# Kernel optimization log

Measured on AMD Instinct MI355X. Metric: run time of the kernel, lower is better.

Reference implementation:

```python
import jax, jax.numpy as jnp
import numpy as np

N_NODES = 100000
N_EDGES = 1600000
IN_DIM = 192   # n_shapes(64) * n_dims(3)
H1, H2 = 64, 32


def _glorot(key, shape):
    lim = np.sqrt(6.0 / (shape[0] + shape[1])).astype(np.float32)
    return jax.random.uniform(key, shape, jnp.float32, -lim, lim)


def setup_inputs() -> dict:
    key = jax.random.key(0)
    ks = jax.random.split(key, 8)
    verts = jax.random.normal(ks[0], (N_NODES, IN_DIM), jnp.float32)
    edges = jax.random.randint(ks[1], (N_EDGES, 2), 0, N_NODES)
    return {
        "verts": verts,
        "edges": edges,
        "W0_1": _glorot(ks[2], (IN_DIM, H1)),
        "W1_1": _glorot(ks[3], (IN_DIM, H1)),
        "b1": jnp.zeros((H1,), jnp.float32),
        "W0_2": _glorot(ks[4], (H1, H2)),
        "W1_2": _glorot(ks[5], (H1, H2)),
        "b2": jnp.zeros((H2,), jnp.float32),
    }


def cheb_conv(x, src, dst, W0, W1, b, n):
    # ChebConv K=2 with lambda_max=2: L_hat = -D^{-1/2} A D^{-1/2} (zero diagonal)
    deg = jax.ops.segment_sum(jnp.ones(src.shape, x.dtype), src, num_segments=n)
    d_inv = jnp.where(deg > 0, jax.lax.rsqrt(jnp.maximum(deg, 1.0)), 0.0)
    norm = -d_inv[src] * d_inv[dst]                      # [E]
    Tx1 = jax.ops.segment_sum(norm[:, None] * x[src], dst, num_segments=n)  # [n,F]
    return x @ W0 + Tx1 @ W1 + b


def reference(verts, edges, W0_1, W1_1, b1, W0_2, W1_2, b2):
    n = verts.shape[0]
    src, dst = edges[:, 0], edges[:, 1]  # edge_index rows after edges.t()
    x = jax.nn.relu(cheb_conv(verts, src, dst, W0_1, W1_1, b1, n))
    return cheb_conv(x, src, dst, W0_2, W1_2, b2, n)
```

## Files before the change

### kernel.cpp

```cpp
#include <hip/hip_runtime.h>

#define N_NODES 100000
#define N_EDGES 1600000
#define IN_DIM  192
#define H1      64
#define H2      32
#define NBKT    391
#define CAP_D   4608
#define K1GRID  2345

typedef __attribute__((ext_vector_type(8))) short short8;
typedef __attribute__((ext_vector_type(4))) float f32x4;

__device__ inline short f2bf(float f) {
    union { float f; unsigned u; } v; v.f = f;
    unsigned r = (v.u + 0x7FFFu + ((v.u >> 16) & 1u)) >> 16;
    return (short)r;
}
__device__ inline float bf2f(unsigned short s) {
    union { unsigned u; float f; } v; v.u = ((unsigned)s) << 16;
    return v.f;
}

__global__ __launch_bounds__(1024) void init_kernel(int* __restrict__ bucket_next) {
    int i = threadIdx.x;
    bucket_next[i] = (i & 511) * CAP_D;
}

__global__ __launch_bounds__(256) void prep_w_kernel(
    const float* __restrict__ W0_1, const float* __restrict__ W1_1,
    const float* __restrict__ W0_2, const float* __restrict__ W1_2,
    short* __restrict__ Bt1, short* __restrict__ Bt2) {
    int idx = blockIdx.x * 256 + threadIdx.x;
    if (idx < 128 * IN_DIM) {
        int n = idx / IN_DIM, k = idx % IN_DIM;
        float v = (n < H1) ? W0_1[(size_t)k * H1 + n] : W1_1[(size_t)k * H1 + (n - H1)];
        Bt1[idx] = f2bf(v);
    } else {
        int j = idx - 128 * IN_DIM;
        if (j < 64 * H1) {
            int n = j / H1, k = j % H1;
            float v = (n < H2) ? W0_2[(size_t)k * H2 + n] : W1_2[(size_t)k * H2 + (n - H2)];
            Bt2[j] = f2bf(v);
        }
    }
}

__global__ __launch_bounds__(256) void k1_fused(
    const int* __restrict__ edges, int* __restrict__ bucket_next,
    int* __restrict__ bins_dst, unsigned char* __restrict__ bins_src,
    const float* __restrict__ verts, const short* __restrict__ Bt1,
    const float* __restrict__ b1, short* __restrict__ hbase, short* __restrict__ y1b) {
    __shared__ int cntd[512];
    __shared__ int curd[512];
    __shared__ int cnts[512];
    __shared__ int curs[512];
    int b = blockIdx.x;
    int tid = threadIdx.x;
    if (b % 3 == 0) {
        int p = b / 3;
        cntd[tid] = 0; cntd[tid + 256] = 0;
        cnts[tid] = 0; cnts[tid + 256] = 0;
        __syncthreads();
        int ebase = p * 2048 + tid * 8;
        int2 ed[8]; int bd[8], bs[8];
#pragma unroll
        for (int i = 0; i < 8; ++i) {
            int e = ebase + i;
            if (e < N_EDGES) {
                ed[i] = ((const int2*)edges)[e];
                bd[i] = ed[i].y >> 8;
                bs[i] = ed[i].x >> 8;
                atomicAdd(&cntd[bd[i]], 1);
                atomicAdd(&cnts[bs[i]], 1);
            } else { bd[i] = -1; bs[i] = -1; }
        }
        __syncthreads();
        {
            int c;
            c = cntd[tid];       curd[tid]       = (c > 0) ? atomicAdd(&bucket_next[tid], c) : 0;
            c = cntd[tid + 256]; curd[tid + 256] = (c > 0) ? atomicAdd(&bucket_next[tid + 256], c) : 0;
            c = cnts[tid];       curs[tid]       = (c > 0) ? atomicAdd(&bucket_next[512 + tid], c) : 0;
            c = cnts[tid + 256]; curs[tid + 256] = (c > 0) ? atomicAdd(&bucket_next[512 + tid + 256], c) : 0;
        }
        __syncthreads();
#pragma unroll
        for (int i = 0; i < 8; ++i) {
            if (bd[i] >= 0) {
                int sd = atomicAdd(&curd[bd[i]], 1);
                if (sd < (bd[i] + 1) * CAP_D)
                    bins_dst[sd] = ((ed[i].y & 255) << 17) | ed[i].x;
                int ss = atomicAdd(&curs[bs[i]], 1);
                if (ss < (bs[i] + 1) * CAP_D)
                    bins_src[ss] = (unsigned char)(ed[i].x & 255);
            }
        }
        return;
    }
    int g = b - b / 3 - 1;
    int lane = tid & 63;
    int wave = tid >> 6;
    int rowbase = g * 64 + wave * 16;
    int lr = lane & 15;
    int lk = (lane >> 4) * 8;

    int row = rowbase + lr;
    int rc = (row < N_NODES) ? row : (N_NODES - 1);
    const float* p = verts + (size_t)rc * IN_DIM + lk;
    short8 a[6];
#pragma unroll
    for (int ks = 0; ks < 6; ++ks) {
        f32x4 u0 = *(const f32x4*)(p + ks * 32);
        f32x4 u1 = *(const f32x4*)(p + ks * 32 + 4);
        short8 t;
        t[0] = f2bf(u0[0]); t[1] = f2bf(u0[1]); t[2] = f2bf(u0[2]); t[3] = f2bf(u0[3]);
        t[4] = f2bf(u1[0]); t[5] = f2bf(u1[1]); t[6] = f2bf(u1[2]); t[7] = f2bf(u1[3]);
        a[ks] = t;
    }

    f32x4 acc[8] = {};
#pragma unroll
    for (int cf = 0; cf < 8; ++cf) {
        const short* bp = Bt1 + (size_t)(cf * 16 + lr) * IN_DIM + lk;
#pragma unroll
        for (int ks = 0; ks < 6; ++ks) {
            short8 bb = *(const short8*)(bp + ks * 32);
            acc[cf] = __builtin_amdgcn_mfma_f32_16x16x32_bf16(a[ks], bb, acc[cf], 0, 0, 0);
        }
    }

    int srow = (lane >> 4) * 4;
#pragma unroll
    for (int cf = 0; cf < 8; ++cf) {
        int colc = cf * 16 + lr;
        float bias = (colc < H1) ? b1[colc] : 0.f;
#pragma unroll
        for (int r = 0; r < 4; ++r) {
            int orow = rowbase + srow + r;
            if (orow < N_NODES) {
                float v = acc[cf][r];
                if (colc < H1) hbase[(size_t)orow * H1 + colc] = f2bf(v + bias);
                else           y1b[(size_t)orow * H1 + (colc - H1)] = f2bf(v);
            }
        }
    }
}

__global__ __launch_bounds__(256) void csr_kernel(
    const int* __restrict__ bins_dst, const unsigned char* __restrict__ bins_src,
    const int* __restrict__ bucket_next, float* __restrict__ dinv,
    int* __restrict__ row_beg, int* __restrict__ row_end, int* __restrict__ col,
    const unsigned short* __restrict__ y1b, short* __restrict__ y1s) {
    __shared__ int cnt_l[256];
    __shared__ int seg_l[256];
    __shared__ int s[256];
    __shared__ int dcnt[256];
    __shared__ float dinv_l[256];
    int b = blockIdx.x;
    int tid = threadIdx.x;
    int beg = b * CAP_D;
    int filld = bucket_next[b] - beg;
    if (filld > CAP_D) filld = CAP_D;
    int fills = bucket_next[512 + b] - beg;
    if (fills > CAP_D) fills = CAP_D;
    cnt_l[tid] = 0;
    dcnt[tid] = 0;
    __syncthreads();
    for (int i = tid; i < filld; i += 256)
        atomicAdd(&cnt_l[bins_dst[beg + i] >> 17], 1);
    for (int i = tid; i < fills; i += 256)
        atomicAdd(&dcnt[bins_src[beg + i]], 1);
    __syncthreads();
    int v = cnt_l[tid];
    s[tid] = v;
    __syncthreads();
    for (int off = 1; off < 256; off <<= 1) {
        int t = (tid >= off) ? s[tid - off] : 0;
        __syncthreads();
        s[tid] += t;
        __syncthreads();
    }
    int excl = s[tid] - v;
    seg_l[tid] = beg + excl;
    int n = b * 256 + tid;
    int d = dcnt[tid];
    float dv = (d > 0) ? rsqrtf((float)d) : 0.f;
    dinv_l[tid] = dv;
    if (n < N_NODES) {
        row_beg[n] = beg + excl;
        row_end[n] = beg + excl + v;
        dinv[n] = dv;
    }
    __syncthreads();
    for (int i = tid; i < filld; i += 256) {
        int w = bins_dst[beg + i];
        int slot = atomicAdd(&seg_l[w >> 17], 1);
        col[slot] = w & 0x1FFFF;
    }
    int nb = b * 256;
    int nmax = N_NODES - nb; if (nmax > 256) nmax = 256;
    for (int idx = tid; idx < nmax * 8; idx += 256) {
        int r = idx >> 3, j = idx & 7;
        float w = dinv_l[r];
        size_t off = (size_t)(nb + r) * H1 + j * 8;
        short8 vv = *(const short8*)&y1b[off];
        short8 o;
#pragma unroll
        for (int q = 0; q < 8; ++q) o[q] = f2bf(w * bf2f((unsigned short)vv[q]));
        *(short8*)&y1s[off] = o;
    }
}

__global__ __launch_bounds__(256) void gather1_kernel(
    const int* __restrict__ row_beg, const int* __restrict__ row_end,
    const int* __restrict__ col, const float* __restrict__ dinv,
    const unsigned short* __restrict__ hbase, const unsigned short* __restrict__ y1s,
    short* __restrict__ hb) {
    int n = blockIdx.x * 4 + (threadIdx.x >> 6);
    if (n >= N_NODES) return;
    int lane = threadIdx.x & 63;
    int beg = row_beg[n], end = row_end[n];
    float acc = 0.f;
    int i = beg;
    for (; i + 8 <= end; i += 8) {
        int s0 = col[i], s1 = col[i + 1], s2 = col[i + 2], s3 = col[i + 3];
        int s4 = col[i + 4], s5 = col[i + 5], s6 = col[i + 6], s7 = col[i + 7];
        float v0 = bf2f(y1s[(size_t)s0 * H1 + lane]);
        float v1 = bf2f(y1s[(size_t)s1 * H1 + lane]);
        float v2 = bf2f(y1s[(size_t)s2 * H1 + lane]);
        float v3 = bf2f(y1s[(size_t)s3 * H1 + lane]);
        float v4 = bf2f(y1s[(size_t)s4 * H1 + lane]);
        float v5 = bf2f(y1s[(size_t)s5 * H1 + lane]);
        float v6 = bf2f(y1s[(size_t)s6 * H1 + lane]);
        float v7 = bf2f(y1s[(size_t)s7 * H1 + lane]);
        acc += ((v0 + v1) + (v2 + v3)) + ((v4 + v5) + (v6 + v7));
    }
    for (; i + 4 <= end; i += 4) {
        int s0 = col[i], s1 = col[i + 1], s2 = col[i + 2], s3 = col[i + 3];
        float v0 = bf2f(y1s[(size_t)s0 * H1 + lane]);
        float v1 = bf2f(y1s[(size_t)s1 * H1 + lane]);
        float v2 = bf2f(y1s[(size_t)s2 * H1 + lane]);
        float v3 = bf2f(y1s[(size_t)s3 * H1 + lane]);
        acc += (v0 + v1) + (v2 + v3);
    }
    for (; i < end; ++i)
        acc += bf2f(y1s[(size_t)col[i] * H1 + lane]);
    size_t idx = (size_t)n * H1 + lane;
    float hf = bf2f(hbase[idx]) - dinv[n] * acc;
    hb[idx] = f2bf(fmaxf(hf, 0.f));
}

__global__ __launch_bounds__(256) void gemm2_mfma(
    const short* __restrict__ hb, const short* __restrict__ Bt2,
    const float* __restrict__ b2, const float* __restrict__ dinv,
    float* __restrict__ out, short* __restrict__ y2s) {
    int lane = threadIdx.x & 63;
    int wave = threadIdx.x >> 6;
    int rowbase = blockIdx.x * 128 + wave * 32;
    int lr = lane & 15;
    int lk = (lane >> 4) * 8;

    short8 a[2][2];
#pragma unroll
    for (int mr = 0; mr < 2; ++mr) {
        int row = rowbase + mr * 16 + lr;
        int rc = (row < N_NODES) ? row : (N_NODES - 1);
        const short* p = hb + (size_t)rc * H1 + lk;
        a[mr][0] = *(const short8*)(p);
        a[mr][1] = *(const short8*)(p + 32);
    }

    f32x4 acc[2][4] = {};
#pragma unroll
    for (int cf = 0; cf < 4; ++cf) {
        const short* bp = Bt2 + (size_t)(cf * 16 + lr) * H1 + lk;
#pragma unroll
        for (int ks = 0; ks < 2; ++ks) {
            short8 b = *(const short8*)(bp + ks * 32);
            acc[0][cf] = __builtin_amdgcn_mfma_f32_16x16x32_bf16(a[0][ks], b, acc[0][cf], 0, 0, 0);
            acc[1][cf] = __builtin_amdgcn_mfma_f32_16x16x32_bf16(a[1][ks], b, acc[1][cf], 0, 0, 0);
        }
    }

    int srow = (lane >> 4) * 4;
#pragma unroll
    for (int mr = 0; mr < 2; ++mr) {
#pragma unroll
        for (int cf = 0; cf < 4; ++cf) {
            int colc = cf * 16 + lr;
            float bias = (colc < H2) ? b2[colc] : 0.f;
#pragma unroll
            for (int r = 0; r < 4; ++r) {
                int row = rowbase + mr * 16 + srow + r;
                if (row < N_NODES) {
                    float v = acc[mr][cf][r];
                    if (colc < H2) out[(size_t)row * H2 + colc] = v + bias;
                    else           y2s[(size_t)row * H2 + (colc - H2)] = f2bf(dinv[row] * v);
                }
            }
        }
    }
}

__global__ __launch_bounds__(256) void gather2_kernel(
    const int* __restrict__ row_beg, const int* __restrict__ row_end,
    const int* __restrict__ col, const float* __restrict__ dinv,
    const unsigned short* __restrict__ y2s, float* __restrict__ out) {
    int wave = (blockIdx.x * 256 + threadIdx.x) >> 6;
    int lane = threadIdx.x & 63;
    int n = wave * 2 + (lane >> 5);
    if (n >= N_NODES) return;
    int c32 = lane & 31;
    int beg = row_beg[n], end = row_end[n];
    float acc = 0.f;
    int i = beg;
    for (; i + 8 <= end; i += 8) {
        int s0 = col[i], s1 = col[i + 1], s2 = col[i + 2], s3 = col[i + 3];
        int s4 = col[i + 4], s5 = col[i + 5], s6 = col[i + 6], s7 = col[i + 7];
        float v0 = bf2f(y2s[(size_t)s0 * H2 + c32]);
        float v1 = bf2f(y2s[(size_t)s1 * H2 + c32]);
        float v2 = bf2f(y2s[(size_t)s2 * H2 + c32]);
        float v3 = bf2f(y2s[(size_t)s3 * H2 + c32]);
        float v4 = bf2f(y2s[(size_t)s4 * H2 + c32]);
        float v5 = bf2f(y2s[(size_t)s5 * H2 + c32]);
        float v6 = bf2f(y2s[(size_t)s6 * H2 + c32]);
        float v7 = bf2f(y2s[(size_t)s7 * H2 + c32]);
        acc += ((v0 + v1) + (v2 + v3)) + ((v4 + v5) + (v6 + v7));
    }
    for (; i + 4 <= end; i += 4) {
        int s0 = col[i], s1 = col[i + 1], s2 = col[i + 2], s3 = col[i + 3];
        float v0 = bf2f(y2s[(size_t)s0 * H2 + c32]);
        float v1 = bf2f(y2s[(size_t)s1 * H2 + c32]);
        float v2 = bf2f(y2s[(size_t)s2 * H2 + c32]);
        float v3 = bf2f(y2s[(size_t)s3 * H2 + c32]);
        acc += (v0 + v1) + (v2 + v3);
    }
    for (; i < end; ++i)
        acc += bf2f(y2s[(size_t)col[i] * H2 + c32]);
    size_t idx = (size_t)n * H2 + c32;
    out[idx] = out[idx] - dinv[n] * acc;
}

extern "C" void kernel_launch(void* const* d_in, const int* in_sizes, int n_in,
                              void* d_out, int out_size, void* d_ws, size_t ws_size,
                              hipStream_t stream) {
    const float* verts = (const float*)d_in[0];
    const int*   edges = (const int*)  d_in[1];
    const float* W0_1  = (const float*)d_in[2];
    const float* W1_1  = (const float*)d_in[3];
    const float* b1    = (const float*)d_in[4];
    const float* W0_2  = (const float*)d_in[5];
    const float* W1_2  = (const float*)d_in[6];
    const float* b2    = (const float*)d_in[7];
    float* out = (float*)d_out;

    char* ws = (char*)d_ws;
    auto align256 = [](size_t x) { return (x + 255) & ~(size_t)255; };
    size_t o = 0;
    auto alloc = [&](size_t bytes) { size_t r = o; o = align256(o + bytes); return r; };

    int*   bucket_next = (int*)  (ws + alloc((size_t)1024 * 4));
    int*   bins_dst    = (int*)  (ws + alloc((size_t)NBKT * CAP_D * 4));
    unsigned char* bins_src = (unsigned char*)(ws + alloc((size_t)NBKT * CAP_D));
    int*   col         = (int*)  (ws + alloc((size_t)NBKT * CAP_D * 4));
    int*   row_beg     = (int*)  (ws + alloc((size_t)N_NODES * 4));
    int*   row_end     = (int*)  (ws + alloc((size_t)N_NODES * 4));
    float* dinv        = (float*)(ws + alloc((size_t)N_NODES * 4));
    short* Bt1         = (short*)(ws + alloc((size_t)128 * IN_DIM * 2));
    short* Bt2         = (short*)(ws + alloc((size_t)64 * H1 * 2));
    short* hbase       = (short*)(ws + alloc((size_t)N_NODES * H1 * 2));
    short* y1b         = (short*)(ws + alloc((size_t)N_NODES * H1 * 2));
    short* y1s         = (short*)(ws + alloc((size_t)N_NODES * H1 * 2));
    short* hb          = (short*)(ws + alloc((size_t)N_NODES * H1 * 2));
    short* y2s         = (short*)(ws + alloc((size_t)N_NODES * H2 * 2));

    init_kernel  <<<1, 1024, 0, stream>>>(bucket_next);
    prep_w_kernel<<<(128 * IN_DIM + 64 * H1 + 255) / 256, 256, 0, stream>>>(W0_1, W1_1, W0_2, W1_2, Bt1, Bt2);

    k1_fused  <<<K1GRID, 256, 0, stream>>>(edges, bucket_next, bins_dst, bins_src,
                                           verts, Bt1, b1, hbase, y1b);
    csr_kernel<<<NBKT, 256, 0, stream>>>(bins_dst, bins_src, bucket_next, dinv,
                                         row_beg, row_end, col,
                                         (const unsigned short*)y1b, y1s);

    gather1_kernel<<<(N_NODES + 3) / 4, 256, 0, stream>>>(row_beg, row_end, col, dinv,
                                                          (const unsigned short*)hbase,
                                                          (const unsigned short*)y1s, hb);
    gemm2_mfma    <<<(N_NODES + 127) / 128, 256, 0, stream>>>(hb, Bt2, b2, dinv, out, y2s);
    gather2_kernel<<<(N_NODES + 7) / 8, 256, 0, stream>>>(row_beg, row_end, col, dinv,
                                                          (const unsigned short*)y2s, out);
}
```

Baseline: 206.4 us.

## Fuse layer-1 gather with layer-2 GEMM and merge init into weight prep

Merges the first-layer neighbor gather and the second-layer MFMA GEMM into one kernel. Each block gathers 16 nodes into shared memory and immediately runs the 16x64 GEMM, which removes the hb intermediate's global write and read plus one launch. It also folds bucket initialisation into the weight-prep kernel, dropping another launch. The edge-binning blocks in k1 now each handle 8192 edges, reading edges twice rather than keeping them in registers, with fewer partition blocks interleaved among the GEMM blocks. The trade-offs are less parallelism in the binning phase and a block-wide sync between the irregular gather and the GEMM.

```diff
diff --git a/kernel.cpp b/kernel.cpp
--- a/kernel.cpp
+++ b/kernel.cpp
@@ -7,7 +7,8 @@
 #define H2      32
 #define NBKT    391
 #define CAP_D   4608
-#define K1GRID  2345
+#define NP1     196
+#define K1GRID  1759
 
 typedef __attribute__((ext_vector_type(8))) short short8;
 typedef __attribute__((ext_vector_type(4))) float f32x4;
@@ -22,15 +23,14 @@
     return v.f;
 }
 
-__global__ __launch_bounds__(1024) void init_kernel(int* __restrict__ bucket_next) {
-    int i = threadIdx.x;
-    bucket_next[i] = (i & 511) * CAP_D;
-}
-
 __global__ __launch_bounds__(256) void prep_w_kernel(
     const float* __restrict__ W0_1, const float* __restrict__ W1_1,
     const float* __restrict__ W0_2, const float* __restrict__ W1_2,
-    short* __restrict__ Bt1, short* __restrict__ Bt2) {
+    short* __restrict__ Bt1, short* __restrict__ Bt2, int* __restrict__ bucket_next) {
+    if (blockIdx.x == 0) {
+        for (int i = threadIdx.x; i < 1024; i += 256)
+            bucket_next[i] = (i & 511) * CAP_D;
+    }
     int idx = blockIdx.x * 256 + threadIdx.x;
     if (idx < 128 * IN_DIM) {
         int n = idx / IN_DIM, k = idx % IN_DIM;
@@ -57,23 +57,24 @@
     __shared__ int curs[512];
     int b = blockIdx.x;
     int tid = threadIdx.x;
-    if (b % 3 == 0) {
-        int p = b / 3;
+    if (b % 9 == 0) {
+        int p = b / 9;
         cntd[tid] = 0; cntd[tid + 256] = 0;
         cnts[tid] = 0; cnts[tid + 256] = 0;
         __syncthreads();
-        int ebase = p * 2048 + tid * 8;
-        int2 ed[8]; int bd[8], bs[8];
-#pragma unroll
-        for (int i = 0; i < 8; ++i) {
-            int e = ebase + i;
-            if (e < N_EDGES) {
-                ed[i] = ((const int2*)edges)[e];
-                bd[i] = ed[i].y >> 8;
-                bs[i] = ed[i].x >> 8;
-                atomicAdd(&cntd[bd[i]], 1);
-                atomicAdd(&cnts[bs[i]], 1);
-            } else { bd[i] = -1; bs[i] = -1; }
+        const int2* e2 = (const int2*)edges;
+        int base = p * 8192;
+        for (int c = 0; c < 4; ++c) {
+            int ebase = base + c * 2048 + tid * 8;
+#pragma unroll
+            for (int i = 0; i < 8; ++i) {
+                int e = ebase + i;
+                if (e < N_EDGES) {
+                    int2 ed = e2[e];
+                    atomicAdd(&cntd[ed.y >> 8], 1);
+                    atomicAdd(&cnts[ed.x >> 8], 1);
+                }
+            }
         }
         __syncthreads();
         {
@@ -84,20 +85,27 @@
             c = cnts[tid + 256]; curs[tid + 256] = (c > 0) ? atomicAdd(&bucket_next[512 + tid + 256], c) : 0;
         }
         __syncthreads();
-#pragma unroll
-        for (int i = 0; i < 8; ++i) {
-            if (bd[i] >= 0) {
-                int sd = atomicAdd(&curd[bd[i]], 1);
-                if (sd < (bd[i] + 1) * CAP_D)
-                    bins_dst[sd] = ((ed[i].y & 255) << 17) | ed[i].x;
-                int ss = atomicAdd(&curs[bs[i]], 1);
-                if (ss < (bs[i] + 1) * CAP_D)
-                    bins_src[ss] = (unsigned char)(ed[i].x & 255);
+        for (int c = 0; c < 4; ++c) {
+            int ebase = base + c * 2048 + tid * 8;
+#pragma unroll
+            for (int i = 0; i < 8; ++i) {
+                int e = ebase + i;
+                if (e < N_EDGES) {
+                    int2 ed = e2[e];
+                    int bd = ed.y >> 8;
+                    int sd = atomicAdd(&curd[bd], 1);
+                    if (sd < (bd + 1) * CAP_D)
+                        bins_dst[sd] = ((ed.y & 255) << 17) | ed.x;
+                    int bs = ed.x >> 8;
+                    int ss = atomicAdd(&curs[bs], 1);
+                    if (ss < (bs + 1) * CAP_D)
+                        bins_src[ss] = (unsigned char)(ed.x & 255);
+                }
             }
         }
         return;
     }
-    int g = b - b / 3 - 1;
+    int g = b - b / 9 - 1;
     int lane = tid & 63;
     int wave = tid >> 6;
     int rowbase = g * 64 + wave * 16;
@@ -211,94 +219,66 @@
     }
 }
 
-__global__ __launch_bounds__(256) void gather1_kernel(
+__global__ __launch_bounds__(256) void g1g2_kernel(
     const int* __restrict__ row_beg, const int* __restrict__ row_end,
     const int* __restrict__ col, const float* __restrict__ dinv,
     const unsigned short* __restrict__ hbase, const unsigned short* __restrict__ y1s,
-    short* __restrict__ hb) {
-    int n = blockIdx.x * 4 + (threadIdx.x >> 6);
-    if (n >= N_NODES) return;
-    int lane = threadIdx.x & 63;
-    int beg = row_beg[n], end = row_end[n];
-    float acc = 0.f;
-    int i = beg;
-    for (; i + 8 <= end; i += 8) {
-        int s0 = col[i], s1 = col[i + 1], s2 = col[i + 2], s3 = col[i + 3];
-        int s4 = col[i + 4], s5 = col[i + 5], s6 = col[i + 6], s7 = col[i + 7];
-        float v0 = bf2f(y1s[(size_t)s0 * H1 + lane]);
-        float v1 = bf2f(y1s[(size_t)s1 * H1 + lane]);
-        float v2 = bf2f(y1s[(size_t)s2 * H1 + lane]);
-        float v3 = bf2f(y1s[(size_t)s3 * H1 + lane]);
-        float v4 = bf2f(y1s[(size_t)s4 * H1 + lane]);
-        float v5 = bf2f(y1s[(size_t)s5 * H1 + lane]);
-        float v6 = bf2f(y1s[(size_t)s6 * H1 + lane]);
-        float v7 = bf2f(y1s[(size_t)s7 * H1 + lane]);
-        acc += ((v0 + v1) + (v2 + v3)) + ((v4 + v5) + (v6 + v7));
-    }
-    for (; i + 4 <= end; i += 4) {
-        int s0 = col[i], s1 = col[i + 1], s2 = col[i + 2], s3 = col[i + 3];
-        float v0 = bf2f(y1s[(size_t)s0 * H1 + lane]);
-        float v1 = bf2f(y1s[(size_t)s1 * H1 + lane]);
-        float v2 = bf2f(y1s[(size_t)s2 * H1 + lane]);
-        float v3 = bf2f(y1s[(size_t)s3 * H1 + lane]);
-        acc += (v0 + v1) + (v2 + v3);
-    }
-    for (; i < end; ++i)
-        acc += bf2f(y1s[(size_t)col[i] * H1 + lane]);
-    size_t idx = (size_t)n * H1 + lane;
-    float hf = bf2f(hbase[idx]) - dinv[n] * acc;
-    hb[idx] = f2bf(fmaxf(hf, 0.f));
-}
-
-__global__ __launch_bounds__(256) void gemm2_mfma(
-    const short* __restrict__ hb, const short* __restrict__ Bt2,
-    const float* __restrict__ b2, const float* __restrict__ dinv,
+    const short* __restrict__ Bt2, const float* __restrict__ b2,
     float* __restrict__ out, short* __restrict__ y2s) {
-    int lane = threadIdx.x & 63;
-    int wave = threadIdx.x >> 6;
-    int rowbase = blockIdx.x * 128 + wave * 32;
+    __shared__ short hb_l[16][68];
+    int tid = threadIdx.x, lane = tid & 63, wv = tid >> 6;
+    int nb = blockIdx.x * 16;
+    for (int j = 0; j < 4; ++j) {
+        int n = nb + wv * 4 + j;
+        int beg = row_beg[n], end = row_end[n];
+        float acc = 0.f;
+        int i = beg;
+        for (; i + 8 <= end; i += 8) {
+            int s0 = col[i], s1 = col[i + 1], s2 = col[i + 2], s3 = col[i + 3];
+            int s4 = col[i + 4], s5 = col[i + 5], s6 = col[i + 6], s7 = col[i + 7];
+            float v0 = bf2f(y1s[(size_t)s0 * H1 + lane]);
+            float v1 = bf2f(y1s[(size_t)s1 * H1 + lane]);
+            float v2 = bf2f(y1s[(size_t)s2 * H1 + lane]);
+            float v3 = bf2f(y1s[(size_t)s3 * H1 + lane]);
+            float v4 = bf2f(y1s[(size_t)s4 * H1 + lane]);
+            float v5 = bf2f(y1s[(size_t)s5 * H1 + lane]);
+            float v6 = bf2f(y1s[(size_t)s6 * H1 + lane]);
+            float v7 = bf2f(y1s[(size_t)s7 * H1 + lane]);
+            acc += ((v0 + v1) + (v2 + v3)) + ((v4 + v5) + (v6 + v7));
+        }
+        for (; i + 4 <= end; i += 4) {
+            int s0 = col[i], s1 = col[i + 1], s2 = col[i + 2], s3 = col[i + 3];
+            float v0 = bf2f(y1s[(size_t)s0 * H1 + lane]);
+            float v1 = bf2f(y1s[(size_t)s1 * H1 + lane]);
+            float v2 = bf2f(y1s[(size_t)s2 * H1 + lane]);
+            float v3 = bf2f(y1s[(size_t)s3 * H1 + lane]);
+            acc += (v0 + v1) + (v2 + v3);
+        }
+        for (; i < end; ++i)
+            acc += bf2f(y1s[(size_t)col[i] * H1 + lane]);
+        float hf = bf2f(hbase[(size_t)n * H1 + lane]) - dinv[n] * acc;
+        hb_l[wv * 4 + j][lane] = f2bf(fmaxf(hf, 0.f));
+    }
+    __syncthreads();
     int lr = lane & 15;
     int lk = (lane >> 4) * 8;
-
-    short8 a[2][2];
-#pragma unroll
-    for (int mr = 0; mr < 2; ++mr) {
-        int row = rowbase + mr * 16 + lr;
-        int rc = (row < N_NODES) ? row : (N_NODES - 1);
-        const short* p = hb + (size_t)rc * H1 + lk;
-        a[mr][0] = *(const short8*)(p);
-        a[mr][1] = *(const short8*)(p + 32);
-    }
-
-    f32x4 acc[2][4] = {};
-#pragma unroll
-    for (int cf = 0; cf < 4; ++cf) {
-        const short* bp = Bt2 + (size_t)(cf * 16 + lr) * H1 + lk;
-#pragma unroll
-        for (int ks = 0; ks < 2; ++ks) {
-            short8 b = *(const short8*)(bp + ks * 32);
-            acc[0][cf] = __builtin_amdgcn_mfma_f32_16x16x32_bf16(a[0][ks], b, acc[0][cf], 0, 0, 0);
-            acc[1][cf] = __builtin_amdgcn_mfma_f32_16x16x32_bf16(a[1][ks], b, acc[1][cf], 0, 0, 0);
-        }
-    }
-
+    short8 a0 = *(const short8*)&hb_l[lr][lk];
+    short8 a1 = *(const short8*)&hb_l[lr][32 + lk];
+    const short* bp = Bt2 + (size_t)(wv * 16 + lr) * H1 + lk;
+    short8 b0 = *(const short8*)(bp);
+    short8 b1 = *(const short8*)(bp + 32);
+    f32x4 acc2 = {};
+    acc2 = __builtin_amdgcn_mfma_f32_16x16x32_bf16(a0, b0, acc2, 0, 0, 0);
+    acc2 = __builtin_amdgcn_mfma_f32_16x16x32_bf16(a1, b1, acc2, 0, 0, 0);
     int srow = (lane >> 4) * 4;
-#pragma unroll
-    for (int mr = 0; mr < 2; ++mr) {
-#pragma unroll
-        for (int cf = 0; cf < 4; ++cf) {
-            int colc = cf * 16 + lr;
-            float bias = (colc < H2) ? b2[colc] : 0.f;
-#pragma unroll
-            for (int r = 0; r < 4; ++r) {
-                int row = rowbase + mr * 16 + srow + r;
-                if (row < N_NODES) {
-                    float v = acc[mr][cf][r];
-                    if (colc < H2) out[(size_t)row * H2 + colc] = v + bias;
-                    else           y2s[(size_t)row * H2 + (colc - H2)] = f2bf(dinv[row] * v);
-                }
-            }
-        }
+    int colc = wv * 16 + lr;
+    float bias = (colc < H2) ? b2[colc] : 0.f;
+#pragma unroll
+    for (int r = 0; r < 4; ++r) {
+        int n = nb + srow + r;
+        float v = acc2[r];
+        if (colc < H2) out[(size_t)n * H2 + colc] = v + bias;
+        else           y2s[(size_t)n * H2 + (colc - H2)] = f2bf(dinv[n] * v);
     }
 }
 
@@ -371,11 +351,9 @@
     short* hbase       = (short*)(ws + alloc((size_t)N_NODES * H1 * 2));
     short* y1b         = (short*)(ws + alloc((size_t)N_NODES * H1 * 2));
     short* y1s         = (short*)(ws + alloc((size_t)N_NODES * H1 * 2));
-    short* hb          = (short*)(ws + alloc((size_t)N_NODES * H1 * 2));
     short* y2s         = (short*)(ws + alloc((size_t)N_NODES * H2 * 2));
 
-    init_kernel  <<<1, 1024, 0, stream>>>(bucket_next);
-    prep_w_kernel<<<(128 * IN_DIM + 64 * H1 + 255) / 256, 256, 0, stream>>>(W0_1, W1_1, W0_2, W1_2, Bt1, Bt2);
+    prep_w_kernel<<<112, 256, 0, stream>>>(W0_1, W1_1, W0_2, W1_2, Bt1, Bt2, bucket_next);
 
     k1_fused  <<<K1GRID, 256, 0, stream>>>(edges, bucket_next, bins_dst, bins_src,
                                            verts, Bt1, b1, hbase, y1b);
@@ -383,10 +361,10 @@
                                          row_beg, row_end, col,
                                          (const unsigned short*)y1b, y1s);
 
-    gather1_kernel<<<(N_NODES + 3) / 4, 256, 0, stream>>>(row_beg, row_end, col, dinv,
-                                                          (const unsigned short*)hbase,
-                                                          (const unsigned short*)y1s, hb);
-    gemm2_mfma    <<<(N_NODES + 127) / 128, 256, 0, stream>>>(hb, Bt2, b2, dinv, out, y2s);
+    g1g2_kernel<<<N_NODES / 16, 256, 0, stream>>>(row_beg, row_end, col, dinv,
+                                                  (const unsigned short*)hbase,
+                                                  (const unsigned short*)y1s,
+                                                  Bt2, b2, out, y2s);
     gather2_kernel<<<(N_NODES + 7) / 8, 256, 0, stream>>>(row_beg, row_end, col, dinv,
                                                           (const unsigned short*)y2s, out);
 }
```

Measured after the change: 210.3 us. Within noise of the previous version (+1.9%).
